# Performance work log

Measured on AMD Instinct MI355X. Metric: run time of the kernel, lower is better.

## Reference

```python
import jax, jax.numpy as jnp
import numpy as np

HIDDEN = 3072
INTER = 8192  # intermediate size; gate_up rows = 2*INTER
B, S = 4, 2048


def dequant_linear(x, w_int, scales):
    # w_int: [out, in] int8-valued, scales: [out] per-output-channel
    # y = x @ (w_int * scales[:, None]).T  computed as (x @ w_int.T) * scales
    y = jnp.einsum('bsh,oh->bso', x, w_int.astype(x.dtype))
    return y * scales


def setup_inputs() -> dict:
    key = jax.random.key(0)
    k1, k2, k3, k4, k5 = jax.random.split(key, 5)
    x = jax.random.normal(k1, (B, S, HIDDEN), dtype=jnp.float32)
    gate_up_w = jax.random.randint(k2, (2 * INTER, HIDDEN), 0, 127, dtype=jnp.int32)
    gate_up_scales = jax.random.uniform(k3, (2 * INTER,), dtype=jnp.float32) * 0.02
    down_w = jax.random.randint(k4, (HIDDEN, INTER), 0, 127, dtype=jnp.int32)
    down_scales = jax.random.uniform(k5, (HIDDEN,), dtype=jnp.float32) * 0.02
    return {
        'x': x,
        'gate_up_w': gate_up_w,
        'gate_up_scales': gate_up_scales,
        'down_w': down_w,
        'down_scales': down_scales,
    }


def reference(x, gate_up_w, gate_up_scales, down_w, down_scales):
    up_states = dequant_linear(x, gate_up_w, gate_up_scales)  # [B,S,2*INTER]
    gate, up = jnp.split(up_states, 2, axis=-1)               # chunk(2, dim=-1)
    hidden = jax.nn.silu(gate) * up                           # [B,S,INTER]
    out = dequant_linear(hidden, down_w, down_scales)         # [B,S,HIDDEN]
    return out
```

## Files before the change

### kernel.cpp

```cpp
#include <hip/hip_runtime.h>
#include <cstdint>
#include <cstddef>

constexpr int HID  = 3072;
constexpr int ITR  = 8192;
constexpr int MTOK = 8192;

constexpr int BM = 128, BN = 128;

typedef __bf16 bf16x8 __attribute__((ext_vector_type(8)));
typedef float  f32x4  __attribute__((ext_vector_type(4)));
typedef int    i32x4  __attribute__((ext_vector_type(4)));


__device__ inline unsigned short f2bf(float f) {
  unsigned int u = __float_as_uint(f);
  u = (u + 0x7FFFu + ((u >> 16) & 1u)) >> 16;
  return (unsigned short)u;
}

__device__ inline void gl2lds16(const void* g, void* l) {
  __builtin_amdgcn_global_load_lds(
      (const __attribute__((address_space(1))) unsigned int*)(uintptr_t)g,
      (__attribute__((address_space(3))) unsigned int*)(unsigned int)(uintptr_t)l,
      16, 0, 0);
}


__global__ __launch_bounds__(256) void quant_x(
    const float* __restrict__ x, signed char* __restrict__ xq,
    float* __restrict__ qs) {
  const int row = blockIdx.x;
  const int t = threadIdx.x;
  const int wave = t >> 6, lane = t & 63;
  const float4* xr = (const float4*)(x + (size_t)row * HID);
  float4 v[3];
  float m = 0.f;
#pragma unroll
  for (int k = 0; k < 3; k++) {
    v[k] = xr[t + 256 * k];
    m = fmaxf(m, fmaxf(fmaxf(fabsf(v[k].x), fabsf(v[k].y)),
                       fmaxf(fabsf(v[k].z), fabsf(v[k].w))));
  }
#pragma unroll
  for (int off = 32; off >= 1; off >>= 1) m = fmaxf(m, __shfl_down(m, off));
  __shared__ float wm[4];
  if (lane == 0) wm[wave] = m;
  __syncthreads();
  const float am = fmaxf(fmaxf(wm[0], wm[1]), fmaxf(wm[2], wm[3]));
  const float inv = (am > 1e-30f) ? 127.f / am : 0.f;
  if (t == 0) qs[row] = (am > 1e-30f) ? am / 127.f : 1.f;
  int* out = (int*)(xq + (size_t)row * HID);
#pragma unroll
  for (int k = 0; k < 3; k++) {
    int r0 = __float2int_rn(v[k].x * inv);
    int r1 = __float2int_rn(v[k].y * inv);
    int r2 = __float2int_rn(v[k].z * inv);
    int r3 = __float2int_rn(v[k].w * inv);
    out[t + 256 * k] =
        (r0 & 255) | ((r1 & 255) << 8) | ((r2 & 255) << 16) | ((r3 & 255) << 24);
  }
}

__global__ __launch_bounds__(256) void cvt_w1_i8(
    const int* __restrict__ in, signed char* __restrict__ out) {
  const int nw = 2 * ITR * (HID / 4);
  int i = blockIdx.x * 256 + threadIdx.x;
  if (i >= nw) return;
  const int R  = i / (HID / 4);
  const int c4 = i % (HID / 4);
  const int q = R >> 5, rm = R & 31;
  const int orig = (rm < 16) ? (q * 16 + rm) : (ITR + q * 16 + (rm - 16));
  int4 w = ((const int4*)(in + (size_t)orig * HID))[c4];
  ((int*)out)[(size_t)R * (HID / 4) + c4] =
      (w.x & 255) | ((w.y & 255) << 8) | ((w.z & 255) << 16) | ((w.w & 255) << 24);
}

__global__ __launch_bounds__(256) void cvt_w2_i8(
    const int* __restrict__ in, signed char* __restrict__ out) {
  const int nw = HID * (ITR / 4);
  int i = blockIdx.x * 256 + threadIdx.x;
  if (i >= nw) return;
  int4 w = ((const int4*)in)[i];
  ((int*)out)[i] =
      (w.x & 255) | ((w.y & 255) << 8) | ((w.z & 255) << 16) | ((w.w & 255) << 24);
}

__global__ __launch_bounds__(256) void quant_h(
    const unsigned short* __restrict__ h, signed char* __restrict__ hq,
    float* __restrict__ qh) {
  const int row = blockIdx.x;
  const int t = threadIdx.x;
  const int wave = t >> 6, lane = t & 63;
  const uint4* hr = (const uint4*)(h + (size_t)row * ITR);
  uint4 v[4];
  float f[32];
  float m = 0.f;
#pragma unroll
  for (int k = 0; k < 4; k++) {
    v[k] = hr[t + 256 * k];
    const unsigned int w[4] = {v[k].x, v[k].y, v[k].z, v[k].w};
#pragma unroll
    for (int j = 0; j < 4; j++) {
      float lo = __uint_as_float(w[j] << 16);
      float hi = __uint_as_float(w[j] & 0xFFFF0000u);
      f[k * 8 + 2 * j]     = lo;
      f[k * 8 + 2 * j + 1] = hi;
      m = fmaxf(m, fmaxf(fabsf(lo), fabsf(hi)));
    }
  }
#pragma unroll
  for (int off = 32; off >= 1; off >>= 1) m = fmaxf(m, __shfl_down(m, off));
  __shared__ float wm[4];
  if (lane == 0) wm[wave] = m;
  __syncthreads();
  const float am = fmaxf(fmaxf(wm[0], wm[1]), fmaxf(wm[2], wm[3]));
  const float inv = (am > 1e-30f) ? 127.f / am : 0.f;
  if (t == 0) qh[row] = (am > 1e-30f) ? am / 127.f : 1.f;
  int* out = (int*)(hq + (size_t)row * ITR);
#pragma unroll
  for (int k = 0; k < 4; k++) {
#pragma unroll
    for (int j = 0; j < 2; j++) {
      int r0 = __float2int_rn(f[k * 8 + 4 * j]     * inv);
      int r1 = __float2int_rn(f[k * 8 + 4 * j + 1] * inv);
      int r2 = __float2int_rn(f[k * 8 + 4 * j + 2] * inv);
      int r3 = __float2int_rn(f[k * 8 + 4 * j + 3] * inv);
      out[(t + 256 * k) * 2 + j] =
          (r0 & 255) | ((r1 & 255) << 8) | ((r2 & 255) << 16) | ((r3 & 255) << 24);
    }
  }
}

__global__ __launch_bounds__(256, 2) void gemm1_i8(
    const signed char* __restrict__ A, const signed char* __restrict__ B,
    const float* __restrict__ qs, const float* __restrict__ scales,
    unsigned short* __restrict__ Hout) {
  const int K = HID;
  const int tid  = threadIdx.x;
  const int wave = tid >> 6;
  const int lane = tid & 63;

  const int PN = 32, MB = MTOK / BM;
  const int bid = blockIdx.x;
  const int panel = bid / (PN * MB);
  const int rem = bid - panel * (PN * MB);
  const int nb = panel * PN + (rem % PN);
  const int mb = rem / PN;
  const int m0 = mb * BM;
  const int n0 = nb * BN;

  __shared__ __align__(16) signed char sA[BM * 64];
  __shared__ __align__(16) signed char sB[BN * 64];

  const int srow  = wave * 16 + (lane >> 2);
  const int chunk = (lane & 3) ^ ((lane >> 3) & 3);
  const signed char* Ag = A + (size_t)(m0 + srow) * K + chunk * 16;
  const signed char* Bg = B + (size_t)(n0 + srow) * K + chunk * 16;

  i32x4 acc[4][4];
#pragma unroll
  for (int i = 0; i < 4; i++)
#pragma unroll
    for (int j = 0; j < 4; j++) acc[i][j] = (i32x4){0, 0, 0, 0};

  const int wr = wave >> 1, wc = wave & 1;
  const int ml = lane & 15;
  const int q  = lane >> 4;
  const int slot = (q ^ ((ml >> 1) & 3)) * 16;

  for (int k0 = 0; k0 < K; k0 += 64) {
    gl2lds16(Ag,                  &sA[(wave * 16) * 64]);
    gl2lds16(Ag + (size_t)64 * K, &sA[(wave * 16 + 64) * 64]);
    gl2lds16(Bg,                  &sB[(wave * 16) * 64]);
    gl2lds16(Bg + (size_t)64 * K, &sB[(wave * 16 + 64) * 64]);
    Ag += 64; Bg += 64;
    __syncthreads();

    i32x4 av[4], bv[4];
#pragma unroll
    for (int i = 0; i < 4; i++)
      av[i] = *(const i32x4*)&sA[(wr * 64 + i * 16 + ml) * 64 + slot];
#pragma unroll
    for (int j = 0; j < 4; j++)
      bv[j] = *(const i32x4*)&sB[(wc * 64 + j * 16 + ml) * 64 + slot];
#pragma unroll
    for (int i = 0; i < 4; i++)
#pragma unroll
      for (int j = 0; j < 4; j++)
        acc[i][j] = __builtin_amdgcn_mfma_i32_16x16x64_i8(av[i], bv[j], acc[i][j], 0, 0, 0);
    __syncthreads();
  }

#pragma unroll
  for (int jp = 0; jp < 2; jp++) {
    const int hcol = (n0 + wc * 64) / 2 + jp * 16 + ml;
    const float sg = scales[hcol];
    const float su = scales[ITR + hcol];
#pragma unroll
    for (int i = 0; i < 4; i++) {
      const int mrow = m0 + wr * 64 + i * 16 + q * 4;
#pragma unroll
      for (int r = 0; r < 4; r++) {
        const float rowqs = qs[mrow + r];
        float g = (float)acc[i][2 * jp][r] * sg * rowqs;
        float u = (float)acc[i][2 * jp + 1][r] * su * rowqs;
        float h = (g / (1.f + __expf(-g))) * u;
        Hout[(size_t)(mrow + r) * ITR + hcol] = f2bf(h);
      }
    }
  }
}

__global__ __launch_bounds__(256, 2) void gemm2_i8(
    const signed char* __restrict__ A, const signed char* __restrict__ B,
    const float* __restrict__ qh, const float* __restrict__ scales,
    float* __restrict__ Cout) {
  const int K = ITR, N = HID;
  const int tid  = threadIdx.x;
  const int wave = tid >> 6;
  const int lane = tid & 63;
  const int m0 = blockIdx.y * BM;
  const int n0 = blockIdx.x * BN;

  __shared__ __align__(16) signed char sA[BM * 64];
  __shared__ __align__(16) signed char sB[BN * 64];

  const int srow  = wave * 16 + (lane >> 2);
  const int chunk = (lane & 3) ^ ((lane >> 3) & 3);
  const signed char* Ag = A + (size_t)(m0 + srow) * K + chunk * 16;
  const signed char* Bg = B + (size_t)(n0 + srow) * K + chunk * 16;

  i32x4 acc[4][4];
#pragma unroll
  for (int i = 0; i < 4; i++)
#pragma unroll
    for (int j = 0; j < 4; j++) acc[i][j] = (i32x4){0, 0, 0, 0};

  const int wr = wave >> 1, wc = wave & 1;
  const int ml = lane & 15;
  const int q  = lane >> 4;
  const int slot = (q ^ ((ml >> 1) & 3)) * 16;

  for (int k0 = 0; k0 < K; k0 += 64) {
    gl2lds16(Ag,                  &sA[(wave * 16) * 64]);
    gl2lds16(Ag + (size_t)64 * K, &sA[(wave * 16 + 64) * 64]);
    gl2lds16(Bg,                  &sB[(wave * 16) * 64]);
    gl2lds16(Bg + (size_t)64 * K, &sB[(wave * 16 + 64) * 64]);
    Ag += 64; Bg += 64;
    __syncthreads();

    i32x4 av[4], bv[4];
#pragma unroll
    for (int i = 0; i < 4; i++)
      av[i] = *(const i32x4*)&sA[(wr * 64 + i * 16 + ml) * 64 + slot];
#pragma unroll
    for (int j = 0; j < 4; j++)
      bv[j] = *(const i32x4*)&sB[(wc * 64 + j * 16 + ml) * 64 + slot];
#pragma unroll
    for (int i = 0; i < 4; i++)
#pragma unroll
      for (int j = 0; j < 4; j++)
        acc[i][j] = __builtin_amdgcn_mfma_i32_16x16x64_i8(av[i], bv[j], acc[i][j], 0, 0, 0);
    __syncthreads();
  }

#pragma unroll
  for (int j = 0; j < 4; j++) {
    const int n = n0 + wc * 64 + j * 16 + ml;
    const float sn = scales[n];
#pragma unroll
    for (int i = 0; i < 4; i++) {
      const int mrow = m0 + wr * 64 + i * 16 + q * 4;
#pragma unroll
      for (int r = 0; r < 4; r++) {
        Cout[(size_t)(mrow + r) * N + n] = (float)acc[i][j][r] * sn * qh[mrow + r];
      }
    }
  }
}


extern "C" void kernel_launch(void* const* d_in, const int* in_sizes, int n_in,
                              void* d_out, int out_size, void* d_ws, size_t ws_size,
                              hipStream_t stream) {
  const float* x  = (const float*)d_in[0];
  const int*   w1 = (const int*)d_in[1];
  const float* s1 = (const float*)d_in[2];
  const int*   w2 = (const int*)d_in[3];
  const float* s2 = (const float*)d_in[4];
  float* out = (float*)d_out;

  signed char* xq  = (signed char*)d_ws;
  float* qs        = (float*)(xq + (size_t)MTOK * HID);
  signed char* w1q = (signed char*)(qs + MTOK);
  signed char* w2q = w1q + (size_t)2 * ITR * HID;
  unsigned short* hid = (unsigned short*)(w2q + (size_t)HID * ITR);
  signed char* hq  = (signed char*)(hid + (size_t)MTOK * ITR);
  float* qh        = (float*)(hq + (size_t)MTOK * ITR);

  quant_x<<<MTOK, 256, 0, stream>>>(x, xq, qs);
  {
    int nw = 2 * ITR * (HID / 4);
    cvt_w1_i8<<<(nw + 255) / 256, 256, 0, stream>>>(w1, w1q);
  }
  {
    int nw = HID * (ITR / 4);
    cvt_w2_i8<<<(nw + 255) / 256, 256, 0, stream>>>(w2, w2q);
  }

  {
    unsigned nblocks = (2 * ITR / BN) * (MTOK / BM);
    gemm1_i8<<<nblocks, 256, 0, stream>>>(xq, w1q, qs, s1, hid);
  }
  quant_h<<<MTOK, 256, 0, stream>>>(hid, hq, qh);
  {
    dim3 grid(HID / BN, MTOK / BM);
    gemm2_i8<<<grid, 256, 0, stream>>>(hq, w2q, qh, s2, out);
  }
}
```

Measured before the change: 1.143 ms.

## Rewrite int8 GEMMs with 256x256 tiles, triple-buffered LDS pipeline, XCD-aware block swizzle

Both int8 GEMM kernels move from 128x128 tiles with 256 threads to 256x256 tiles with 512 threads (8 waves, 8x4 MFMA accumulators per wave). A three-stage LDS ring is prefetched two k-steps ahead with global_load_lds, and the MFMA work is split into two halves interleaved with loads, using explicit barriers, waitcnts and s_setprio. Block IDs are remapped across the 8 XCDs and grouped into panels for L2 reuse. The goal is to hide global-load latency and raise arithmetic intensity, at the cost of 96KB of LDS per block, more registers, and a fragile hand-written synchronisation scheme.

Result: faster. 1.072 ms (-6.2%).

```diff
diff --git a/kernel.cpp b/kernel.cpp
--- a/kernel.cpp
+++ b/kernel.cpp
@@ -6,11 +6,7 @@
 constexpr int ITR  = 8192;
 constexpr int MTOK = 8192;
 
-constexpr int BM = 128, BN = 128;
-
-typedef __bf16 bf16x8 __attribute__((ext_vector_type(8)));
-typedef float  f32x4  __attribute__((ext_vector_type(4)));
-typedef int    i32x4  __attribute__((ext_vector_type(4)));
+typedef int i32x4 __attribute__((ext_vector_type(4)));
 
 
 __device__ inline unsigned short f2bf(float f) {
@@ -132,64 +128,105 @@
   }
 }
 
-__global__ __launch_bounds__(256, 2) void gemm1_i8(
+
+__global__ __launch_bounds__(512, 2) void gemm1_i8_v2(
     const signed char* __restrict__ A, const signed char* __restrict__ B,
     const float* __restrict__ qs, const float* __restrict__ scales,
     unsigned short* __restrict__ Hout) {
-  const int K = HID;
-  const int tid  = threadIdx.x;
-  const int wave = tid >> 6;
-  const int lane = tid & 63;
-
-  const int PN = 32, MB = MTOK / BM;
+  constexpr int K = HID, NT = K / 64;
+  constexpr int MB = MTOK / 256;
+  constexpr int NB = (2 * ITR) / 256;
+  constexpr int PN = 4;
+
+  const int tid = threadIdx.x;
+  const int wave = tid >> 6, lane = tid & 63;
+
   const int bid = blockIdx.x;
-  const int panel = bid / (PN * MB);
-  const int rem = bid - panel * (PN * MB);
-  const int nb = panel * PN + (rem % PN);
+  const int wg = (bid & 7) * (MB * NB / 8) + (bid >> 3);
+  const int panel = wg / (PN * MB);
+  const int rem = wg - panel * (PN * MB);
+  const int nb = panel * PN + (rem & (PN - 1));
   const int mb = rem / PN;
-  const int m0 = mb * BM;
-  const int n0 = nb * BN;
-
-  __shared__ __align__(16) signed char sA[BM * 64];
-  __shared__ __align__(16) signed char sB[BN * 64];
-
-  const int srow  = wave * 16 + (lane >> 2);
+  const int m0 = mb * 256;
+  const int n0 = nb * 256;
+
+  __shared__ __align__(16) signed char sA[3][256 * 64];
+  __shared__ __align__(16) signed char sB[3][256 * 64];
+
+  const int srow  = wave * 32 + (lane >> 2);
   const int chunk = (lane & 3) ^ ((lane >> 3) & 3);
   const signed char* Ag = A + (size_t)(m0 + srow) * K + chunk * 16;
   const signed char* Bg = B + (size_t)(n0 + srow) * K + chunk * 16;
-
-  i32x4 acc[4][4];
-#pragma unroll
-  for (int i = 0; i < 4; i++)
+  const int ldsw = (wave * 32) * 64;
+
+  auto stageA = [&](int ks, int b) {
+    gl2lds16(Ag + ks * 64,          &sA[b][ldsw]);
+    gl2lds16(Ag + ks * 64 + 16 * K, &sA[b][ldsw + 1024]);
+  };
+  auto stageB = [&](int ks, int b) {
+    gl2lds16(Bg + ks * 64,          &sB[b][ldsw]);
+    gl2lds16(Bg + ks * 64 + 16 * K, &sB[b][ldsw + 1024]);
+  };
+
+  i32x4 acc[8][4];
+#pragma unroll
+  for (int i = 0; i < 8; i++)
 #pragma unroll
     for (int j = 0; j < 4; j++) acc[i][j] = (i32x4){0, 0, 0, 0};
 
-  const int wr = wave >> 1, wc = wave & 1;
+  const int wr = wave >> 2, wc = wave & 3;
   const int ml = lane & 15;
   const int q  = lane >> 4;
   const int slot = (q ^ ((ml >> 1) & 3)) * 16;
 
-  for (int k0 = 0; k0 < K; k0 += 64) {
-    gl2lds16(Ag,                  &sA[(wave * 16) * 64]);
-    gl2lds16(Ag + (size_t)64 * K, &sA[(wave * 16 + 64) * 64]);
-    gl2lds16(Bg,                  &sB[(wave * 16) * 64]);
-    gl2lds16(Bg + (size_t)64 * K, &sB[(wave * 16 + 64) * 64]);
-    Ag += 64; Bg += 64;
-    __syncthreads();
-
+  stageA(0, 0); stageB(0, 0);
+  stageA(1, 1); stageB(1, 1);
+  asm volatile("s_waitcnt vmcnt(4)" ::: "memory");
+  __builtin_amdgcn_s_barrier();
+
+  int cur = 0, sb = 2;
+  for (int t = 0; t < NT; ++t) {
+    int ks = t + 2; if (ks >= NT) ks -= NT;
+    const signed char* a_ = sA[cur];
+    const signed char* b_ = sB[cur];
     i32x4 av[4], bv[4];
 #pragma unroll
-    for (int i = 0; i < 4; i++)
-      av[i] = *(const i32x4*)&sA[(wr * 64 + i * 16 + ml) * 64 + slot];
-#pragma unroll
     for (int j = 0; j < 4; j++)
-      bv[j] = *(const i32x4*)&sB[(wc * 64 + j * 16 + ml) * 64 + slot];
+      bv[j] = *(const i32x4*)&b_[(wc * 64 + j * 16 + ml) * 64 + slot];
+#pragma unroll
+    for (int i = 0; i < 4; i++)
+      av[i] = *(const i32x4*)&a_[(wr * 128 + i * 16 + ml) * 64 + slot];
+    stageA(ks, sb);
+    __builtin_amdgcn_s_barrier();
+    asm volatile("s_waitcnt lgkmcnt(0)" ::: "memory");
+    __builtin_amdgcn_sched_barrier(0);
+    __builtin_amdgcn_s_setprio(1);
 #pragma unroll
     for (int i = 0; i < 4; i++)
 #pragma unroll
       for (int j = 0; j < 4; j++)
         acc[i][j] = __builtin_amdgcn_mfma_i32_16x16x64_i8(av[i], bv[j], acc[i][j], 0, 0, 0);
-    __syncthreads();
+    __builtin_amdgcn_s_setprio(0);
+    __builtin_amdgcn_s_barrier();
+    i32x4 av2[4];
+#pragma unroll
+    for (int i = 0; i < 4; i++)
+      av2[i] = *(const i32x4*)&a_[(wr * 128 + (i + 4) * 16 + ml) * 64 + slot];
+    stageB(ks, sb);
+    asm volatile("s_waitcnt vmcnt(4)" ::: "memory");
+    __builtin_amdgcn_s_barrier();
+    asm volatile("s_waitcnt lgkmcnt(0)" ::: "memory");
+    __builtin_amdgcn_sched_barrier(0);
+    __builtin_amdgcn_s_setprio(1);
+#pragma unroll
+    for (int i = 0; i < 4; i++)
+#pragma unroll
+      for (int j = 0; j < 4; j++)
+        acc[i + 4][j] = __builtin_amdgcn_mfma_i32_16x16x64_i8(av2[i], bv[j], acc[i + 4][j], 0, 0, 0);
+    __builtin_amdgcn_s_setprio(0);
+    __builtin_amdgcn_s_barrier();
+    cur++; if (cur == 3) cur = 0;
+    sb++;  if (sb == 3)  sb = 0;
   }
 
 #pragma unroll
@@ -198,8 +235,8 @@
     const float sg = scales[hcol];
     const float su = scales[ITR + hcol];
 #pragma unroll
-    for (int i = 0; i < 4; i++) {
-      const int mrow = m0 + wr * 64 + i * 16 + q * 4;
+    for (int i = 0; i < 8; i++) {
+      const int mrow = m0 + wr * 128 + i * 16 + q * 4;
 #pragma unroll
       for (int r = 0; r < 4; r++) {
         const float rowqs = qs[mrow + r];
@@ -212,57 +249,104 @@
   }
 }
 
-__global__ __launch_bounds__(256, 2) void gemm2_i8(
+__global__ __launch_bounds__(512, 2) void gemm2_i8_v2(
     const signed char* __restrict__ A, const signed char* __restrict__ B,
     const float* __restrict__ qh, const float* __restrict__ scales,
     float* __restrict__ Cout) {
-  const int K = ITR, N = HID;
-  const int tid  = threadIdx.x;
-  const int wave = tid >> 6;
-  const int lane = tid & 63;
-  const int m0 = blockIdx.y * BM;
-  const int n0 = blockIdx.x * BN;
-
-  __shared__ __align__(16) signed char sA[BM * 64];
-  __shared__ __align__(16) signed char sB[BN * 64];
-
-  const int srow  = wave * 16 + (lane >> 2);
+  constexpr int K = ITR, N = HID, NT = K / 64;
+  constexpr int MB = MTOK / 256;
+  constexpr int NB = N / 256;
+  constexpr int PN = 2;
+
+  const int tid = threadIdx.x;
+  const int wave = tid >> 6, lane = tid & 63;
+
+  const int bid = blockIdx.x;
+  const int wg = (bid & 7) * (MB * NB / 8) + (bid >> 3);
+  const int panel = wg / (PN * MB);
+  const int rem = wg - panel * (PN * MB);
+  const int nb = panel * PN + (rem & (PN - 1));
+  const int mb = rem / PN;
+  const int m0 = mb * 256;
+  const int n0 = nb * 256;
+
+  __shared__ __align__(16) signed char sA[3][256 * 64];
+  __shared__ __align__(16) signed char sB[3][256 * 64];
+
+  const int srow  = wave * 32 + (lane >> 2);
   const int chunk = (lane & 3) ^ ((lane >> 3) & 3);
   const signed char* Ag = A + (size_t)(m0 + srow) * K + chunk * 16;
   const signed char* Bg = B + (size_t)(n0 + srow) * K + chunk * 16;
-
-  i32x4 acc[4][4];
-#pragma unroll
-  for (int i = 0; i < 4; i++)
+  const int ldsw = (wave * 32) * 64;
+
+  auto stageA = [&](int ks, int b) {
+    gl2lds16(Ag + ks * 64,          &sA[b][ldsw]);
+    gl2lds16(Ag + ks * 64 + 16 * K, &sA[b][ldsw + 1024]);
+  };
+  auto stageB = [&](int ks, int b) {
+    gl2lds16(Bg + ks * 64,          &sB[b][ldsw]);
+    gl2lds16(Bg + ks * 64 + 16 * K, &sB[b][ldsw + 1024]);
+  };
+
+  i32x4 acc[8][4];
+#pragma unroll
+  for (int i = 0; i < 8; i++)
 #pragma unroll
     for (int j = 0; j < 4; j++) acc[i][j] = (i32x4){0, 0, 0, 0};
 
-  const int wr = wave >> 1, wc = wave & 1;
+  const int wr = wave >> 2, wc = wave & 3;
   const int ml = lane & 15;
   const int q  = lane >> 4;
   const int slot = (q ^ ((ml >> 1) & 3)) * 16;
 
-  for (int k0 = 0; k0 < K; k0 += 64) {
-    gl2lds16(Ag,                  &sA[(wave * 16) * 64]);
-    gl2lds16(Ag + (size_t)64 * K, &sA[(wave * 16 + 64) * 64]);
-    gl2lds16(Bg,                  &sB[(wave * 16) * 64]);
-    gl2lds16(Bg + (size_t)64 * K, &sB[(wave * 16 + 64) * 64]);
-    Ag += 64; Bg += 64;
-    __syncthreads();
-
+  stageA(0, 0); stageB(0, 0);
+  stageA(1, 1); stageB(1, 1);
+  asm volatile("s_waitcnt vmcnt(4)" ::: "memory");
+  __builtin_amdgcn_s_barrier();
+
+  int cur = 0, sb = 2;
+  for (int t = 0; t < NT; ++t) {
+    int ks = t + 2; if (ks >= NT) ks -= NT;
+    const signed char* a_ = sA[cur];
+    const signed char* b_ = sB[cur];
     i32x4 av[4], bv[4];
 #pragma unroll
-    for (int i = 0; i < 4; i++)
-      av[i] = *(const i32x4*)&sA[(wr * 64 + i * 16 + ml) * 64 + slot];
-#pragma unroll
     for (int j = 0; j < 4; j++)
-      bv[j] = *(const i32x4*)&sB[(wc * 64 + j * 16 + ml) * 64 + slot];
+      bv[j] = *(const i32x4*)&b_[(wc * 64 + j * 16 + ml) * 64 + slot];
+#pragma unroll
+    for (int i = 0; i < 4; i++)
+      av[i] = *(const i32x4*)&a_[(wr * 128 + i * 16 + ml) * 64 + slot];
+    stageA(ks, sb);
+    __builtin_amdgcn_s_barrier();
+    asm volatile("s_waitcnt lgkmcnt(0)" ::: "memory");
+    __builtin_amdgcn_sched_barrier(0);
+    __builtin_amdgcn_s_setprio(1);
 #pragma unroll
     for (int i = 0; i < 4; i++)
 #pragma unroll
       for (int j = 0; j < 4; j++)
         acc[i][j] = __builtin_amdgcn_mfma_i32_16x16x64_i8(av[i], bv[j], acc[i][j], 0, 0, 0);
-    __syncthreads();
+    __builtin_amdgcn_s_setprio(0);
+    __builtin_amdgcn_s_barrier();
+    i32x4 av2[4];
+#pragma unroll
+    for (int i = 0; i < 4; i++)
+      av2[i] = *(const i32x4*)&a_[(wr * 128 + (i + 4) * 16 + ml) * 64 + slot];
+    stageB(ks, sb);
+    asm volatile("s_waitcnt vmcnt(4)" ::: "memory");
+    __builtin_amdgcn_s_barrier();
+    asm volatile("s_waitcnt lgkmcnt(0)" ::: "memory");
+    __builtin_amdgcn_sched_barrier(0);
+    __builtin_amdgcn_s_setprio(1);
+#pragma unroll
+    for (int i = 0; i < 4; i++)
+#pragma unroll
+      for (int j = 0; j < 4; j++)
+        acc[i + 4][j] = __builtin_amdgcn_mfma_i32_16x16x64_i8(av2[i], bv[j], acc[i + 4][j], 0, 0, 0);
+    __builtin_amdgcn_s_setprio(0);
+    __builtin_amdgcn_s_barrier();
+    cur++; if (cur == 3) cur = 0;
+    sb++;  if (sb == 3)  sb = 0;
   }
 
 #pragma unroll
@@ -270,8 +354,8 @@
     const int n = n0 + wc * 64 + j * 16 + ml;
     const float sn = scales[n];
 #pragma unroll
-    for (int i = 0; i < 4; i++) {
-      const int mrow = m0 + wr * 64 + i * 16 + q * 4;
+    for (int i = 0; i < 8; i++) {
+      const int mrow = m0 + wr * 128 + i * 16 + q * 4;
 #pragma unroll
       for (int r = 0; r < 4; r++) {
         Cout[(size_t)(mrow + r) * N + n] = (float)acc[i][j][r] * sn * qh[mrow + r];
@@ -310,12 +394,12 @@
   }
 
   {
-    unsigned nblocks = (2 * ITR / BN) * (MTOK / BM);
-    gemm1_i8<<<nblocks, 256, 0, stream>>>(xq, w1q, qs, s1, hid);
+    unsigned nblocks = (2 * ITR / 256) * (MTOK / 256);
+    gemm1_i8_v2<<<nblocks, 512, 0, stream>>>(xq, w1q, qs, s1, hid);
   }
   quant_h<<<MTOK, 256, 0, stream>>>(hid, hq, qh);
   {
-    dim3 grid(HID / BN, MTOK / BM);
-    gemm2_i8<<<grid, 256, 0, stream>>>(hq, w2q, qh, s2, out);
-  }
-}
+    unsigned nblocks = (HID / 256) * (MTOK / 256);
+    gemm2_i8_v2<<<nblocks, 512, 0, stream>>>(hq, w2q, qh, s2, out);
+  }
+}
```
